# Optimization experiments

Hardware: AMD Instinct MI355X
Metric: run time of the kernel (lower is better)

Reference implementation:

```python
import jax, jax.numpy as jnp
import numpy as np

N = 20000
E = 200000
F_IN = 23
H1, C1 = 8, 120   # gat1: heads=8, out=120 -> concat dim 960
D1 = H1 * C1
H2, C2 = 1, 1     # gat2: heads=1, out=1
NEG_SLOPE = 0.2


def _gatv2_layer(x, src, dst, Wl, bl, Wr, br, att, bias, H, C):
    """GATv2Conv (PyG semantics, share_weights=False, concat).
    x: [N, F]; src/dst: [E] (messages flow src -> dst).
    """
    n = x.shape[0]
    xl = (x @ Wl + bl).reshape(n, H, C)   # source-side transform
    xr = (x @ Wr + br).reshape(n, H, C)   # target-side transform
    # per-edge attention logit: a^T LeakyReLU(xl[j] + xr[i])
    s = jax.nn.leaky_relu(xl[src] + xr[dst], NEG_SLOPE)   # [E, H, C]
    e = jnp.einsum('ehc,hc->eh', s, att)                  # [E, H]
    # segment softmax over incoming edges of each target node
    m = jax.ops.segment_max(e, dst, num_segments=n)       # [N, H]
    ex = jnp.exp(e - m[dst])
    denom = jax.ops.segment_sum(ex, dst, num_segments=n)  # [N, H]
    alpha = ex / (denom[dst] + 1e-16)                     # [E, H]
    out = jax.ops.segment_sum(alpha[:, :, None] * xl[src], dst, num_segments=n)
    return out.reshape(n, H * C) + bias


def setup_inputs() -> dict:
    key = jax.random.key(0)
    ks = jax.random.split(key, 14)
    x = jax.random.normal(ks[0], (N, F_IN), dtype=jnp.float32)
    edge_index = jax.random.randint(ks[1], (2, E), 0, N, dtype=jnp.int64)
    def lin(k, fin, fout):
        return jax.random.normal(k, (fin, fout), dtype=jnp.float32) / np.float32(np.sqrt(fin))
    return {
        'x': x,
        'edge_index': edge_index,
        'W1l': lin(ks[2], F_IN, D1), 'b1l': jnp.zeros((D1,), jnp.float32),
        'W1r': lin(ks[3], F_IN, D1), 'b1r': jnp.zeros((D1,), jnp.float32),
        'att1': jax.random.normal(ks[4], (H1, C1), dtype=jnp.float32) / np.float32(np.sqrt(C1)),
        'bias1': jnp.zeros((D1,), jnp.float32),
        'W2l': lin(ks[5], D1, H2 * C2), 'b2l': jnp.zeros((H2 * C2,), jnp.float32),
        'W2r': lin(ks[6], D1, H2 * C2), 'b2r': jnp.zeros((H2 * C2,), jnp.float32),
        'att2': jax.random.normal(ks[7], (H2, C2), dtype=jnp.float32),
        'bias2': jnp.zeros((H2 * C2,), jnp.float32),
    }


def reference(x, edge_index, W1l, b1l, W1r, b1r, att1, bias1,
              W2l, b2l, W2r, b2r, att2, bias2):
    # add self loops (PyG GATv2Conv default add_self_loops=True)
    loops = jnp.arange(N, dtype=edge_index.dtype)
    src = jnp.concatenate([edge_index[0], loops])
    dst = jnp.concatenate([edge_index[1], loops])
    h = _gatv2_layer(x, src, dst, W1l, b1l, W1r, b1r, att1, bias1, H1, C1)
    h = jax.nn.relu(h)
    # F.dropout treated as identity (deterministic/eval reference)
    out = _gatv2_layer(h, src, dst, W2l, b2l, W2r, b2r, att2, bias2, H2, C2)
    return out  # [N, 1]
```

## Files before the change

kernel.cpp:

```cpp
#include <hip/hip_runtime.h>
#include <hip/hip_fp16.h>
#include <math.h>

#define N    20000
#define E    200000
#define EP   220000
#define F_IN 23
#define D1   960
#define H1   8
#define C1   120
#define KPL  15
#define PC   16
#define ROW  1024

typedef _Float16 f16x2 __attribute__((ext_vector_type(2)));

__device__ inline float fdot2(__half2 a, __half2 b, float c) {
#if __has_builtin(__builtin_amdgcn_fdot2)
  f16x2 av, bv;
  __builtin_memcpy(&av, &a, 4);
  __builtin_memcpy(&bv, &b, 4);
  return __builtin_amdgcn_fdot2(av, bv, c, false);
#else
  float2 af = __half22float2(a), bf = __half22float2(b);
  return fmaf(af.x, bf.x, fmaf(af.y, bf.y, c));
#endif
}

__device__ inline __half2 hmax2(__half2 a, __half2 b) {
  f16x2 av, bv;
  __builtin_memcpy(&av, &a, 4);
  __builtin_memcpy(&bv, &b, 4);
  f16x2 rv = __builtin_elementwise_max(av, bv);
  __half2 r;
  __builtin_memcpy(&r, &rv, 4);
  return r;
}

#define T1_BLOCKS 500
#define T1_NPB    40
#define T1_TILE   20
#define CNT_BLOCKS 430
__global__ __launch_bounds__(512, 4)
void k_t1_count(const float* __restrict__ x,
                const float* __restrict__ W1l, const float* __restrict__ b1l,
                const float* __restrict__ W1r, const float* __restrict__ b1r,
                __half* __restrict__ xl1, __half* __restrict__ xr1,
                const int* __restrict__ ei, int* __restrict__ deg) {
  int tid = threadIdx.x;
  if (blockIdx.x >= T1_BLOCKS) {
    int id = (blockIdx.x - T1_BLOCKS) * 512 + tid;
    if (id < EP) {
      int dst = (id < E) ? ei[E + id] : (id - E);
      atomicAdd(&deg[dst], 1);
    }
    return;
  }
  int rlane = tid >> 3, kp = tid & 7;
  int c0 = (rlane >> 3) * C1 + (rlane & 7) * KPL + 2 * kp;
  bool hasK1 = (kp < 7);
  float wl0[F_IN], wl1[F_IN], wr0[F_IN], wr1[F_IN];
#pragma unroll
  for (int f = 0; f < F_IN; f++) {
    wl0[f] = W1l[f * D1 + c0];
    wr0[f] = W1r[f * D1 + c0];
    wl1[f] = hasK1 ? W1l[f * D1 + c0 + 1] : 0.f;
    wr1[f] = hasK1 ? W1r[f * D1 + c0 + 1] : 0.f;
  }
  float bl0 = b1l[c0], br0 = b1r[c0];
  float bl1 = hasK1 ? b1l[c0 + 1] : 0.f;
  float br1 = hasK1 ? b1r[c0 + 1] : 0.f;

  __shared__ float xs[T1_TILE][F_IN];
  int nbase = blockIdx.x * T1_NPB;
  unsigned int* xl1u = (unsigned int*)xl1;
  unsigned int* xr1u = (unsigned int*)xr1;
  for (int t = 0; t < T1_NPB; t += T1_TILE) {
    if (tid < T1_TILE * F_IN) {
      int n = tid / F_IN, f = tid - n * F_IN;
      xs[n][f] = x[(size_t)(nbase + t + n) * F_IN + f];
    }
    __syncthreads();
    for (int n = 0; n < T1_TILE; n++) {
      float a0 = bl0, a1 = bl1, r0 = br0, r1 = br1;
#pragma unroll
      for (int f = 0; f < F_IN; f++) {
        float xv = xs[n][f];
        a0 = fmaf(xv, wl0[f], a0);
        a1 = fmaf(xv, wl1[f], a1);
        r0 = fmaf(xv, wr0[f], r0);
        r1 = fmaf(xv, wr1[f], r1);
      }
      size_t o = (size_t)(nbase + t + n) * 512 + tid;
      unsigned int ul = ((unsigned int)__half_as_ushort(__float2half(a1)) << 16)
                      | __half_as_ushort(__float2half(a0));
      unsigned int ur = ((unsigned int)__half_as_ushort(__float2half(r1)) << 16)
                      | __half_as_ushort(__float2half(r0));
      __builtin_nontemporal_store(ul, &xl1u[o]);
      __builtin_nontemporal_store(ur, &xr1u[o]);
    }
    __syncthreads();
  }
}

#define SC_TOT 20480
__global__ __launch_bounds__(1024)
void k_scan(const int* __restrict__ deg, int* __restrict__ off,
            int* __restrict__ cursor) {
  __shared__ int buf[SC_TOT];
  __shared__ int parts[1024];
  __shared__ int wsum[17];
  int tid = threadIdx.x;
  for (int i = tid; i < SC_TOT; i += 1024) buf[i] = (i < N) ? deg[i] : 0;
  __syncthreads();
  int base = tid * 20;
  int loc[20];
  int run = 0;
#pragma unroll
  for (int e = 0; e < 20; e++) { loc[e] = run; run += buf[base + e]; }
  parts[tid] = run;
  __syncthreads();
  int lane = tid & 63, wid = tid >> 6;
  int v = parts[tid];
  int incl = v;
#pragma unroll
  for (int d = 1; d < 64; d <<= 1) {
    int t = __shfl_up(incl, d, 64);
    if (lane >= d) incl += t;
  }
  if (lane == 63) wsum[wid] = incl;
  __syncthreads();
  if (tid == 0) {
    int acc = 0;
#pragma unroll
    for (int w = 0; w < 16; w++) { int t = wsum[w]; wsum[w] = acc; acc += t; }
    wsum[16] = acc;
  }
  __syncthreads();
  int texcl = incl - v + wsum[wid];
#pragma unroll
  for (int e = 0; e < 20; e++) buf[base + e] = texcl + loc[e];
  __syncthreads();
  for (int i = tid; i < N; i += 1024) {
    int t = buf[i];
    off[i] = t;
    cursor[i] = t;
  }
  if (tid == 0) off[N] = wsum[16];
}

__global__ __launch_bounds__(512)
void k_scatter(const int* __restrict__ ei, int* __restrict__ cursor,
               int* __restrict__ srcs) {
  int id = blockIdx.x * 512 + threadIdx.x;
  if (id >= EP) return;
  int dst, src;
  if (id < E) { dst = ei[E + id]; src = ei[id]; }
  else        { dst = id - E;     src = id - E; }
  int pos = atomicAdd(&cursor[dst], 1);
  srcs[pos] = src;
}

union Rowu {
  uint4 u[2];
  __half2 h[8];
};

__global__ __launch_bounds__(128, 6)
void k_l1agg(const int* __restrict__ off, const int* __restrict__ srcs,
             const __half* __restrict__ xl1, const __half* __restrict__ xr1,
             const float* __restrict__ att1, const float* __restrict__ bias1,
             const float* __restrict__ W2l, const float* __restrict__ b2l,
             const float* __restrict__ W2r, const float* __restrict__ b2r,
             float* __restrict__ xl2, float* __restrict__ xr2) {
  int node = blockIdx.x * 2 + (threadIdx.x >> 6);
  if (node >= N) return;
  int lane = threadIdx.x & 63;
  int cbase = (lane >> 3) * C1 + (lane & 7) * KPL;

  Rowu xr;
  {
    const uint4* rp = (const uint4*)(xr1 + ((size_t)node << 10)) + (lane << 1);
    xr.u[0] = rp[0]; xr.u[1] = rp[1];
  }
  __half2 at2[8];
#pragma unroll
  for (int j = 0; j < 7; j++)
    at2[j] = __floats2half2_rn(att1[cbase + 2 * j], att1[cbase + 2 * j + 1]);
  at2[7] = __floats2half2_rn(att1[cbase + 14], 0.f);

  const __half2 c02 = __float2half2_rn(0.2f);
  __half2 o2[8];
#pragma unroll
  for (int j = 0; j < 8; j++) o2[j] = __float2half2_rn(0.f);
  float m = -INFINITY, d = 0.f;

  int p0 = off[node], p1 = off[node + 1];
  int sA = srcs[p0];
  int sB = srcs[(p0 + 1 < p1) ? p0 + 1 : p1 - 1];
  int sC = srcs[(p0 + 2 < p1) ? p0 + 2 : p1 - 1];
  Rowu rA, rB, rC;
  {
    const uint4* pa = (const uint4*)(xl1 + ((size_t)sA << 10)) + (lane << 1);
    rA.u[0] = pa[0]; rA.u[1] = pa[1];
    const uint4* pb = (const uint4*)(xl1 + ((size_t)sB << 10)) + (lane << 1);
    rB.u[0] = pb[0]; rB.u[1] = pb[1];
    const uint4* pc = (const uint4*)(xl1 + ((size_t)sC << 10)) + (lane << 1);
    rC.u[0] = pc[0]; rC.u[1] = pc[1];
  }

  for (int p = p0; p < p1; p++) {
    Rowu cur = rA;
    rA = rB; rB = rC;
    int pn = (p + 3 < p1) ? p + 3 : p1 - 1;
    int sn = srcs[pn];
    const uint4* np = (const uint4*)(xl1 + ((size_t)sn << 10)) + (lane << 1);
    rC.u[0] = np[0]; rC.u[1] = np[1];

    float pe = 0.f;
#pragma unroll
    for (int j = 0; j < 8; j++) {
      __half2 s = __hadd2(cur.h[j], xr.h[j]);
      __half2 l = hmax2(s, __hmul2(c02, s));
      pe = fdot2(l, at2[j], pe);
    }
    pe += __shfl_xor(pe, 1, 64);
    pe += __shfl_xor(pe, 2, 64);
    pe += __shfl_xor(pe, 4, 64);
    if (pe > m) {
      float sc = __expf(m - pe);
      d *= sc;
      __half2 s2 = __float2half2_rn(sc);
#pragma unroll
      for (int j = 0; j < 8; j++) o2[j] = __hmul2(o2[j], s2);
      m = pe;
    }
    float w = __expf(pe - m);
    d += w;
    __half2 w2 = __float2half2_rn(w);
#pragma unroll
    for (int j = 0; j < 8; j++) o2[j] = __hfma2(w2, cur.h[j], o2[j]);
  }

  float inv = 1.f / (d + 1e-16f);
  float pl = 0.f, pr = 0.f;
#pragma unroll
  for (int j = 0; j < 8; j++) {
    float2 of = __half22float2(o2[j]);
    int k0 = 2 * j;
    float hv = fmaf(of.x, inv, bias1[cbase + k0]);
    hv = fmaxf(hv, 0.f);
    pl = fmaf(hv, W2l[cbase + k0], pl);
    pr = fmaf(hv, W2r[cbase + k0], pr);
    if (j < 7) {
      float hv2 = fmaf(of.y, inv, bias1[cbase + k0 + 1]);
      hv2 = fmaxf(hv2, 0.f);
      pl = fmaf(hv2, W2l[cbase + k0 + 1], pl);
      pr = fmaf(hv2, W2r[cbase + k0 + 1], pr);
    }
  }
#pragma unroll
  for (int dx = 1; dx < 64; dx <<= 1) {
    pl += __shfl_xor(pl, dx, 64);
    pr += __shfl_xor(pr, dx, 64);
  }
  if (lane == 0) {
    xl2[node] = pl + b2l[0];
    xr2[node] = pr + b2r[0];
  }
}

__global__ void k_l2agg(const int* __restrict__ off, const int* __restrict__ srcs,
                        const float* __restrict__ xl2, const float* __restrict__ xr2,
                        const float* __restrict__ att2, const float* __restrict__ bias2,
                        float* __restrict__ out) {
  int node = blockIdx.x * blockDim.x + threadIdx.x;
  if (node >= N) return;
  float xr = xr2[node];
  float a2 = att2[0];
  float m = -INFINITY, d = 0.f, o = 0.f;
  int p1 = off[node + 1];
  for (int p = off[node]; p < p1; p++) {
    float xl = xl2[srcs[p]];
    float s = xl + xr;
    s = fmaxf(s, 0.2f * s);
    float e = s * a2;
    if (e > m) { float sc = __expf(m - e); d *= sc; o *= sc; m = e; }
    float w = __expf(e - m);
    d += w;
    o = fmaf(w, xl, o);
  }
  out[node] = o / (d + 1e-16f) + bias2[0];
}

extern "C" void kernel_launch(void* const* d_in, const int* in_sizes, int n_in,
                              void* d_out, int out_size, void* d_ws, size_t ws_size,
                              hipStream_t stream) {
  const float* x     = (const float*)d_in[0];
  const int*   ei    = (const int*)d_in[1];
  const float* W1l   = (const float*)d_in[2];
  const float* b1l   = (const float*)d_in[3];
  const float* W1r   = (const float*)d_in[4];
  const float* b1r   = (const float*)d_in[5];
  const float* att1  = (const float*)d_in[6];
  const float* bias1 = (const float*)d_in[7];
  const float* W2l   = (const float*)d_in[8];
  const float* b2l   = (const float*)d_in[9];
  const float* W2r   = (const float*)d_in[10];
  const float* b2r   = (const float*)d_in[11];
  const float* att2  = (const float*)d_in[12];
  const float* bias2 = (const float*)d_in[13];
  float* out = (float*)d_out;

  char* ws = (char*)d_ws;
  size_t off_b = 0;
  auto alloc = [&](size_t bytes) {
    size_t cur = off_b;
    off_b += (bytes + 255) & ~(size_t)255;
    return (void*)(ws + cur);
  };
  __half* xl1 = (__half*)alloc((size_t)N * ROW * sizeof(__half));
  __half* xr1 = (__half*)alloc((size_t)N * ROW * sizeof(__half));
  int*   deg  = (int*)alloc((size_t)N * sizeof(int));
  int*   offp = (int*)alloc((size_t)(N + 1) * sizeof(int));
  int*   curs = (int*)alloc((size_t)N * sizeof(int));
  int*   srcs = (int*)alloc((size_t)EP * sizeof(int));
  float* xl2  = (float*)alloc((size_t)N * sizeof(float));
  float* xr2  = (float*)alloc((size_t)N * sizeof(float));
  (void)ws_size; (void)in_sizes; (void)n_in; (void)out_size;

  (void)hipMemsetAsync(deg, 0, (size_t)N * sizeof(int), stream);

  k_t1_count<<<T1_BLOCKS + CNT_BLOCKS, 512, 0, stream>>>(
      x, W1l, b1l, W1r, b1r, xl1, xr1, ei, deg);

  k_scan<<<1, 1024, 0, stream>>>(deg, offp, curs);
  k_scatter<<<(EP + 511) / 512, 512, 0, stream>>>(ei, curs, srcs);

  k_l1agg<<<(N + 1) / 2, 128, 0, stream>>>(
      offp, srcs, xl1, xr1, att1, bias1, W2l, b2l, W2r, b2r, xl2, xr2);

  k_l2agg<<<(N + 255) / 256, 256, 0, stream>>>(
      offp, srcs, xl2, xr2, att2, bias2, out);
}
```

Measured before the change: 158.1 us.

## Fold degree scan into count kernel via last-block pattern and deepen gather prefetch

The separate single-block scan kernel is removed. The last degree-counting block, found through an atomic completion counter, now does the prefix scan over degrees inside the fused transform/count kernel, which saves one launch and its serialization. The layer-1 aggregation now prefetches four neighbor rows instead of three, fetches source indices one step further ahead, and raises the occupancy hint from 6 to 8. The scan now runs on 512 threads with 40 elements each, and the higher occupancy target may force register spills.

```diff
diff --git a/kernel.cpp b/kernel.cpp
--- a/kernel.cpp
+++ b/kernel.cpp
@@ -46,16 +46,70 @@
                 const float* __restrict__ W1l, const float* __restrict__ b1l,
                 const float* __restrict__ W1r, const float* __restrict__ b1r,
                 __half* __restrict__ xl1, __half* __restrict__ xr1,
-                const int* __restrict__ ei, int* __restrict__ deg) {
+                const int* __restrict__ ei, int* __restrict__ deg,
+                int* __restrict__ dcnt,
+                int* __restrict__ off, int* __restrict__ cursor) {
   int tid = threadIdx.x;
+  __shared__ union {
+    float xs[T1_TILE][F_IN];
+    struct { int parts[512]; int wsum[9]; } sc;
+  } sh;
+  __shared__ bool slast;
+
   if (blockIdx.x >= T1_BLOCKS) {
     int id = (blockIdx.x - T1_BLOCKS) * 512 + tid;
     if (id < EP) {
       int dst = (id < E) ? ei[E + id] : (id - E);
       atomicAdd(&deg[dst], 1);
     }
+    __syncthreads();
+    if (tid == 0) {
+      __threadfence();
+      slast = (atomicAdd(dcnt, 1) == CNT_BLOCKS - 1);
+    }
+    __syncthreads();
+    if (!slast) return;
+    int base = tid * 40;
+    int loc[40];
+    int run = 0;
+#pragma unroll
+    for (int e = 0; e < 40; e++) {
+      int i = base + e;
+      int v = (i < N) ? __hip_atomic_load(&deg[i], __ATOMIC_RELAXED,
+                                          __HIP_MEMORY_SCOPE_AGENT)
+                      : 0;
+      loc[e] = run;
+      run += v;
+    }
+    sh.sc.parts[tid] = run;
+    __syncthreads();
+    int lane = tid & 63, wid = tid >> 6;
+    int v = sh.sc.parts[tid];
+    int incl = v;
+#pragma unroll
+    for (int d = 1; d < 64; d <<= 1) {
+      int t = __shfl_up(incl, d, 64);
+      if (lane >= d) incl += t;
+    }
+    if (lane == 63) sh.sc.wsum[wid] = incl;
+    __syncthreads();
+    if (tid == 0) {
+      int acc = 0;
+#pragma unroll
+      for (int w = 0; w < 8; w++) { int t = sh.sc.wsum[w]; sh.sc.wsum[w] = acc; acc += t; }
+      sh.sc.wsum[8] = acc;
+    }
+    __syncthreads();
+    int texcl = incl - v + sh.sc.wsum[wid];
+#pragma unroll
+    for (int e = 0; e < 40; e++) {
+      int i = base + e;
+      if (i < N) { int t = texcl + loc[e]; off[i] = t; cursor[i] = t; }
+    }
+    if (tid == 0) off[N] = sh.sc.wsum[8];
     return;
   }
+
   int rlane = tid >> 3, kp = tid & 7;
   int c0 = (rlane >> 3) * C1 + (rlane & 7) * KPL + 2 * kp;
   bool hasK1 = (kp < 7);
@@ -71,21 +125,20 @@
   float bl1 = hasK1 ? b1l[c0 + 1] : 0.f;
   float br1 = hasK1 ? b1r[c0 + 1] : 0.f;
 
-  __shared__ float xs[T1_TILE][F_IN];
   int nbase = blockIdx.x * T1_NPB;
   unsigned int* xl1u = (unsigned int*)xl1;
   unsigned int* xr1u = (unsigned int*)xr1;
   for (int t = 0; t < T1_NPB; t += T1_TILE) {
     if (tid < T1_TILE * F_IN) {
       int n = tid / F_IN, f = tid - n * F_IN;
-      xs[n][f] = x[(size_t)(nbase + t + n) * F_IN + f];
+      sh.xs[n][f] = x[(size_t)(nbase + t + n) * F_IN + f];
     }
     __syncthreads();
     for (int n = 0; n < T1_TILE; n++) {
       float a0 = bl0, a1 = bl1, r0 = br0, r1 = br1;
 #pragma unroll
       for (int f = 0; f < F_IN; f++) {
-        float xv = xs[n][f];
+        float xv = sh.xs[n][f];
         a0 = fmaf(xv, wl0[f], a0);
         a1 = fmaf(xv, wl1[f], a1);
         r0 = fmaf(xv, wr0[f], r0);
@@ -103,52 +156,6 @@
   }
 }
 
-#define SC_TOT 20480
-__global__ __launch_bounds__(1024)
-void k_scan(const int* __restrict__ deg, int* __restrict__ off,
-            int* __restrict__ cursor) {
-  __shared__ int buf[SC_TOT];
-  __shared__ int parts[1024];
-  __shared__ int wsum[17];
-  int tid = threadIdx.x;
-  for (int i = tid; i < SC_TOT; i += 1024) buf[i] = (i < N) ? deg[i] : 0;
-  __syncthreads();
-  int base = tid * 20;
-  int loc[20];
-  int run = 0;
-#pragma unroll
-  for (int e = 0; e < 20; e++) { loc[e] = run; run += buf[base + e]; }
-  parts[tid] = run;
-  __syncthreads();
-  int lane = tid & 63, wid = tid >> 6;
-  int v = parts[tid];
-  int incl = v;
-#pragma unroll
-  for (int d = 1; d < 64; d <<= 1) {
-    int t = __shfl_up(incl, d, 64);
-    if (lane >= d) incl += t;
-  }
-  if (lane == 63) wsum[wid] = incl;
-  __syncthreads();
-  if (tid == 0) {
-    int acc = 0;
-#pragma unroll
-    for (int w = 0; w < 16; w++) { int t = wsum[w]; wsum[w] = acc; acc += t; }
-    wsum[16] = acc;
-  }
-  __syncthreads();
-  int texcl = incl - v + wsum[wid];
-#pragma unroll
-  for (int e = 0; e < 20; e++) buf[base + e] = texcl + loc[e];
-  __syncthreads();
-  for (int i = tid; i < N; i += 1024) {
-    int t = buf[i];
-    off[i] = t;
-    cursor[i] = t;
-  }
-  if (tid == 0) off[N] = wsum[16];
-}
-
 __global__ __launch_bounds__(512)
 void k_scatter(const int* __restrict__ ei, int* __restrict__ cursor,
                int* __restrict__ srcs) {
@@ -166,7 +173,7 @@
   __half2 h[8];
 };
 
-__global__ __launch_bounds__(128, 6)
+__global__ __launch_bounds__(128, 8)
 void k_l1agg(const int* __restrict__ off, const int* __restrict__ srcs,
              const __half* __restrict__ xl1, const __half* __restrict__ xr1,
              const float* __restrict__ att1, const float* __restrict__ bias1,
@@ -196,26 +203,30 @@
   float m = -INFINITY, d = 0.f;
 
   int p0 = off[node], p1 = off[node + 1];
-  int sA = srcs[p0];
-  int sB = srcs[(p0 + 1 < p1) ? p0 + 1 : p1 - 1];
-  int sC = srcs[(p0 + 2 < p1) ? p0 + 2 : p1 - 1];
-  Rowu rA, rB, rC;
+  int last = p1 - 1;
+  auto rowp = [&](int s) {
+    return (const uint4*)(xl1 + ((size_t)s << 10)) + (lane << 1);
+  };
+  int i1 = (p0 + 1 < p1) ? p0 + 1 : last;
+  int i2 = (p0 + 2 < p1) ? p0 + 2 : last;
+  int i3 = (p0 + 3 < p1) ? p0 + 3 : last;
+  int i4 = (p0 + 4 < p1) ? p0 + 4 : last;
+  Rowu rA, rB, rC, rD;
   {
-    const uint4* pa = (const uint4*)(xl1 + ((size_t)sA << 10)) + (lane << 1);
-    rA.u[0] = pa[0]; rA.u[1] = pa[1];
-    const uint4* pb = (const uint4*)(xl1 + ((size_t)sB << 10)) + (lane << 1);
-    rB.u[0] = pb[0]; rB.u[1] = pb[1];
-    const uint4* pc = (const uint4*)(xl1 + ((size_t)sC << 10)) + (lane << 1);
-    rC.u[0] = pc[0]; rC.u[1] = pc[1];
-  }
+    const uint4* pa = rowp(srcs[p0]); rA.u[0] = pa[0]; rA.u[1] = pa[1];
+    const uint4* pb = rowp(srcs[i1]); rB.u[0] = pb[0]; rB.u[1] = pb[1];
+    const uint4* pc = rowp(srcs[i2]); rC.u[0] = pc[0]; rC.u[1] = pc[1];
+    const uint4* pd = rowp(srcs[i3]); rD.u[0] = pd[0]; rD.u[1] = pd[1];
+  }
+  int sN = srcs[i4];
 
   for (int p = p0; p < p1; p++) {
     Rowu cur = rA;
-    rA = rB; rB = rC;
-    int pn = (p + 3 < p1) ? p + 3 : p1 - 1;
-    int sn = srcs[pn];
-    const uint4* np = (const uint4*)(xl1 + ((size_t)sn << 10)) + (lane << 1);
-    rC.u[0] = np[0]; rC.u[1] = np[1];
+    rA = rB; rB = rC; rC = rD;
+    const uint4* np = rowp(sN);
+    rD.u[0] = np[0]; rD.u[1] = np[1];
+    int pn = (p + 5 < p1) ? p + 5 : last;
+    sN = srcs[pn];
 
     float pe = 0.f;
 #pragma unroll
@@ -321,20 +332,20 @@
   };
   __half* xl1 = (__half*)alloc((size_t)N * ROW * sizeof(__half));
   __half* xr1 = (__half*)alloc((size_t)N * ROW * sizeof(__half));
-  int*   deg  = (int*)alloc((size_t)N * sizeof(int));
+  int*   deg  = (int*)alloc((size_t)(N + 1) * sizeof(int));
   int*   offp = (int*)alloc((size_t)(N + 1) * sizeof(int));
   int*   curs = (int*)alloc((size_t)N * sizeof(int));
   int*   srcs = (int*)alloc((size_t)EP * sizeof(int));
   float* xl2  = (float*)alloc((size_t)N * sizeof(float));
   float* xr2  = (float*)alloc((size_t)N * sizeof(float));
+  int*   dcnt = deg + N;
   (void)ws_size; (void)in_sizes; (void)n_in; (void)out_size;
 
-  (void)hipMemsetAsync(deg, 0, (size_t)N * sizeof(int), stream);
+  (void)hipMemsetAsync(deg, 0, (size_t)(N + 1) * sizeof(int), stream);
 
   k_t1_count<<<T1_BLOCKS + CNT_BLOCKS, 512, 0, stream>>>(
-      x, W1l, b1l, W1r, b1r, xl1, xr1, ei, deg);
-
-  k_scan<<<1, 1024, 0, stream>>>(deg, offp, curs);
+      x, W1l, b1l, W1r, b1r, xl1, xr1, ei, deg, dcnt, offp, curs);
+
   k_scatter<<<(EP + 511) / 512, 512, 0, stream>>>(ei, curs, srcs);
 
   k_l1agg<<<(N + 1) / 2, 128, 0, stream>>>(
```

After: 329.3 us. +108.3%, slower.
